# Optimization experiments

Hardware: AMD Instinct MI355X
Metric: run time of the kernel (lower is better)

Reference implementation:

```python
import jax, jax.numpy as jnp
import numpy as np

NUM_NODES = 100000
FVLEN = 256
HDIM = 256
B = 16384
NNEIGH = 32


def setup_inputs() -> dict:
    key = jax.random.key(0)
    k0, k1, k2, k3, k4 = jax.random.split(key, 5)
    x0 = jax.random.randint(k0, (B,), 0, NUM_NODES)
    x1 = jax.random.randint(k1, (B, NNEIGH), 0, NUM_NODES)
    emb = jax.random.normal(k2, (NUM_NODES, FVLEN), dtype=jnp.float32)
    # xavier_uniform-style init for linear weights
    lim = float(np.sqrt(6.0 / (FVLEN + HDIM)))
    W_self = jax.random.uniform(k3, (HDIM, FVLEN), jnp.float32, -lim, lim)
    W_neigh = jax.random.uniform(k4, (HDIM, FVLEN), jnp.float32, -lim, lim)
    b_self = jnp.zeros((HDIM,), jnp.float32)
    b_neigh = jnp.zeros((HDIM,), jnp.float32)
    return {"x0": x0, "x1": x1, "emb": emb, "W_self": W_self,
            "b_self": b_self, "W_neigh": W_neigh, "b_neigh": b_neigh}


def reference(x0, x1, emb, W_self, b_self, W_neigh, b_neigh):
    # gather self features: [B, F]
    self_feats = emb[x0]
    # gather neighbor features and mean-pool over neighbor axis: [B, F]
    neigh_feats = emb[x1].mean(axis=1)
    # dual linear projections (torch Linear: x @ W.T + b)
    self_out = self_feats @ W_self.T + b_self       # [B, H]
    neigh_out = neigh_feats @ W_neigh.T + b_neigh   # [B, H]
    # concat + relu: [B, 2H]
    return jax.nn.relu(jnp.concatenate([self_out, neigh_out], axis=1))
```

## Files before the change

kernel.cpp:

```cpp
#include <hip/hip_runtime.h>

typedef __attribute__((ext_vector_type(4))) float f32x4;
typedef __attribute__((ext_vector_type(8))) short bf16x8;

#define NN 32
#define FV 256

__device__ __forceinline__ unsigned short bf16_rne(float x) {
    unsigned int u = __float_as_uint(x);
    u += 0x7FFFu + ((u >> 16) & 1u);
    return (unsigned short)(u >> 16);
}
__device__ __forceinline__ float bf16_f(unsigned short h) {
    return __uint_as_float(((unsigned int)h) << 16);
}

__global__ __launch_bounds__(256) void pack_weights(
    const float* __restrict__ Wself, const float* __restrict__ Wneigh,
    unsigned short* __restrict__ wpack)
{
    const float* W = blockIdx.y ? Wneigh : Wself;
    unsigned short* hi = wpack + (size_t)blockIdx.y * 131072;
    unsigned short* lo = hi + 65536;
    int t = blockIdx.x * 256 + threadIdx.x;
    int l = t & 63;
    int ks = (t >> 6) & 7;
    int ct = t >> 9;
    int h = ct * 16 + (l & 15);
    int f0 = ks * 32 + ((l >> 4) << 3);
    const float* src = W + h * 256 + f0;
    f32x4 a = *(const f32x4*)src;
    f32x4 b = *(const f32x4*)(src + 4);
    bf16x8 hv, lv;
#pragma unroll
    for (int e = 0; e < 8; ++e) {
        float x = (e < 4) ? a[e] : b[e - 4];
        unsigned short h16 = bf16_rne(x);
        hv[e] = (short)h16;
        lv[e] = (short)bf16_rne(x - bf16_f(h16));
    }
    *(bf16x8*)(hi + (size_t)t * 8) = hv;
    *(bf16x8*)(lo + (size_t)t * 8) = lv;
}

__global__ __launch_bounds__(256) void gather_pool(
    const int* __restrict__ x0, const int* __restrict__ x1,
    const float* __restrict__ emb, float* __restrict__ out)
{
    int b = blockIdx.x;
    int tid = threadIdx.x;
    int g = tid >> 6, l = tid & 63;
    __shared__ f32x4 red[3][64];

    const int* xr = x1 + b * NN;
    int idx[8];
#pragma unroll
    for (int jj = 0; jj < 8; ++jj) idx[jj] = xr[g + jj * 4];

    int sidx = 0;
    if (g == 0) sidx = x0[b];

    f32x4 acc = {0.f, 0.f, 0.f, 0.f};
#pragma unroll
    for (int jj = 0; jj < 8; ++jj) {
        const f32x4* row = (const f32x4*)(emb + (size_t)idx[jj] * FV);
        acc += row[l];
    }
    f32x4 s = {0.f, 0.f, 0.f, 0.f};
    if (g == 0) s = ((const f32x4*)(emb + (size_t)sidx * FV))[l];

    if (g > 0) red[g - 1][l] = acc;
    __syncthreads();
    if (g == 0) {
        f32x4 p = acc + red[0][l] + red[1][l] + red[2][l];
        p *= (1.0f / 32.0f);
        f32x4* o = (f32x4*)(out + (size_t)b * 512);
        o[l] = s;
        o[64 + l] = p;
    }
}

__global__ __launch_bounds__(256) void dual_gemm(
    const float* X, const unsigned short* __restrict__ wpack,
    const float* __restrict__ bias_self, const float* __restrict__ bias_neigh,
    float* out)
{
    __shared__ short Xh[64 * 256];
    __shared__ short Xl[64 * 256];
    int half = blockIdx.y;
    int b0 = blockIdx.x * 64;
    int tid = threadIdx.x;

    const unsigned short* Whi = wpack + (size_t)half * 131072;
    const unsigned short* Wlo = Whi + 65536;
    const float* bias = half ? bias_neigh : bias_self;

#pragma unroll
    for (int it = 0; it < 8; ++it) {
        int c = it * 256 + tid;
        int row = c >> 5;
        int k8 = c & 31;
        const float* src = X + (size_t)(b0 + row) * 512 + half * 256 + k8 * 8;
        f32x4 v0 = *(const f32x4*)src;
        f32x4 v1 = *(const f32x4*)(src + 4);
        bf16x8 hv, lv;
#pragma unroll
        for (int e = 0; e < 8; ++e) {
            float x = (e < 4) ? v0[e] : v1[e - 4];
            unsigned short h16 = bf16_rne(x);
            hv[e] = (short)h16;
            lv[e] = (short)bf16_rne(x - bf16_f(h16));
        }
        int boff = (row * 512 + k8 * 16) ^ ((row & 7) << 4);
        *(bf16x8*)((char*)Xh + boff) = hv;
        *(bf16x8*)((char*)Xl + boff) = lv;
    }
    __syncthreads();

    int w = tid >> 6, l = tid & 63;
    int mh = w & 1;
    int nh = w >> 1;
    int colq = l & 15;
    int kq = l >> 4;

    f32x4 acc[2][8];
#pragma unroll
    for (int c = 0; c < 8; ++c) {
        int ct = nh * 8 + c;
        float bv = bias[ct * 16 + colq];
#pragma unroll
        for (int m = 0; m < 2; ++m) acc[m][c] = {bv, bv, bv, bv};
    }

#pragma unroll
    for (int ks = 0; ks < 8; ++ks) {
        bf16x8 Ah[2], Al[2];
#pragma unroll
        for (int m = 0; m < 2; ++m) {
            int row = mh * 32 + m * 16 + colq;
            int boff = (row * 512 + ks * 64 + (kq << 4)) ^ ((row & 7) << 4);
            Ah[m] = *(const bf16x8*)((const char*)Xh + boff);
            Al[m] = *(const bf16x8*)((const char*)Xl + boff);
        }
#pragma unroll
        for (int c = 0; c < 8; ++c) {
            int ct = nh * 8 + c;
            size_t fo = ((size_t)(ct * 8 + ks) * 64 + l) * 8;
            bf16x8 Bh = *(const bf16x8*)(Whi + fo);
            bf16x8 Bl = *(const bf16x8*)(Wlo + fo);
#pragma unroll
            for (int m = 0; m < 2; ++m) {
                acc[m][c] = __builtin_amdgcn_mfma_f32_16x16x32_bf16(Ah[m], Bh, acc[m][c], 0, 0, 0);
                acc[m][c] = __builtin_amdgcn_mfma_f32_16x16x32_bf16(Al[m], Bh, acc[m][c], 0, 0, 0);
                acc[m][c] = __builtin_amdgcn_mfma_f32_16x16x32_bf16(Ah[m], Bl, acc[m][c], 0, 0, 0);
            }
        }
    }

#pragma unroll
    for (int m = 0; m < 2; ++m) {
        int rb = mh * 32 + m * 16 + (kq << 2);
#pragma unroll
        for (int c = 0; c < 8; ++c) {
            int col = (nh * 8 + c) * 16 + colq;
            float* o = out + (size_t)(b0 + rb) * 512 + half * 256 + col;
#pragma unroll
            for (int j = 0; j < 4; ++j) {
                o[(size_t)j * 512] = fmaxf(acc[m][c][j], 0.0f);
            }
        }
    }
}

extern "C" void kernel_launch(void* const* d_in, const int* in_sizes, int n_in,
                              void* d_out, int out_size, void* d_ws, size_t ws_size,
                              hipStream_t stream) {
    const int* x0 = (const int*)d_in[0];
    const int* x1 = (const int*)d_in[1];
    const float* emb = (const float*)d_in[2];
    const float* Wself = (const float*)d_in[3];
    const float* bself = (const float*)d_in[4];
    const float* Wneigh = (const float*)d_in[5];
    const float* bneigh = (const float*)d_in[6];
    float* out = (float*)d_out;
    unsigned short* wpack = (unsigned short*)d_ws;

    pack_weights<<<dim3(32, 2), 256, 0, stream>>>(Wself, Wneigh, wpack);
    gather_pool<<<16384, 256, 0, stream>>>(x0, x1, emb, out);
    dual_gemm<<<dim3(256, 2), 256, 0, stream>>>(out, wpack, bself, bneigh, out);
}
```

Measured before the change: 246.4 us.

## Split activations into bf16 hi/lo planes in gather and retile GEMM with LDS-staged weights

The gather kernel now writes the pooled and self features as precomputed bf16 hi/lo planes to workspace instead of fp32 into the output buffer. This removes the fp32 re-read and per-block conversion inside the GEMM. A new GEMM kernel uses 512-thread blocks with 256-row tiles, stages a weight slice in LDS, and reads the A operand directly from global memory. The fast path runs only if the workspace is large enough; otherwise it falls back to the old path, and it adds extra workspace traffic for the intermediate planes.

After: 244.9 us. About the same (-0.6%).

```diff
diff --git a/kernel.cpp b/kernel.cpp
--- a/kernel.cpp
+++ b/kernel.cpp
@@ -2,6 +2,7 @@
 
 typedef __attribute__((ext_vector_type(4))) float f32x4;
 typedef __attribute__((ext_vector_type(8))) short bf16x8;
+typedef __attribute__((ext_vector_type(4))) short bf16x4;
 
 #define NN 32
 #define FV 256
@@ -43,9 +44,10 @@
     *(bf16x8*)(lo + (size_t)t * 8) = lv;
 }
 
-__global__ __launch_bounds__(256) void gather_pool(
+__global__ __launch_bounds__(256) void gather_pool_split(
     const int* __restrict__ x0, const int* __restrict__ x1,
-    const float* __restrict__ emb, float* __restrict__ out)
+    const float* __restrict__ emb,
+    unsigned short* __restrict__ Xhi, unsigned short* __restrict__ Xlo)
 {
     int b = blockIdx.x;
     int tid = threadIdx.x;
@@ -74,13 +76,142 @@
     if (g == 0) {
         f32x4 p = acc + red[0][l] + red[1][l] + red[2][l];
         p *= (1.0f / 32.0f);
-        f32x4* o = (f32x4*)(out + (size_t)b * 512);
+        bf16x4 sh, sl, ph, pl;
+#pragma unroll
+        for (int e = 0; e < 4; ++e) {
+            unsigned short h16 = bf16_rne(s[e]);
+            sh[e] = (short)h16;
+            sl[e] = (short)bf16_rne(s[e] - bf16_f(h16));
+            unsigned short h2 = bf16_rne(p[e]);
+            ph[e] = (short)h2;
+            pl[e] = (short)bf16_rne(p[e] - bf16_f(h2));
+        }
+        size_t base = (size_t)b * 512 + l * 4;
+        *(bf16x4*)(Xhi + base)       = sh;
+        *(bf16x4*)(Xlo + base)       = sl;
+        *(bf16x4*)(Xhi + base + 256) = ph;
+        *(bf16x4*)(Xlo + base + 256) = pl;
+    }
+}
+
+__global__ __launch_bounds__(256) void gather_pool(
+    const int* __restrict__ x0, const int* __restrict__ x1,
+    const float* __restrict__ emb, float* __restrict__ xout)
+{
+    int b = blockIdx.x;
+    int tid = threadIdx.x;
+    int g = tid >> 6, l = tid & 63;
+    __shared__ f32x4 red[3][64];
+
+    const int* xr = x1 + b * NN;
+    int idx[8];
+#pragma unroll
+    for (int jj = 0; jj < 8; ++jj) idx[jj] = xr[g + jj * 4];
+
+    int sidx = 0;
+    if (g == 0) sidx = x0[b];
+
+    f32x4 acc = {0.f, 0.f, 0.f, 0.f};
+#pragma unroll
+    for (int jj = 0; jj < 8; ++jj) {
+        const f32x4* row = (const f32x4*)(emb + (size_t)idx[jj] * FV);
+        acc += row[l];
+    }
+    f32x4 s = {0.f, 0.f, 0.f, 0.f};
+    if (g == 0) s = ((const f32x4*)(emb + (size_t)sidx * FV))[l];
+
+    if (g > 0) red[g - 1][l] = acc;
+    __syncthreads();
+    if (g == 0) {
+        f32x4 p = acc + red[0][l] + red[1][l] + red[2][l];
+        p *= (1.0f / 32.0f);
+        f32x4* o = (f32x4*)(xout + (size_t)b * 512);
         o[l] = s;
         o[64 + l] = p;
     }
 }
 
-__global__ __launch_bounds__(256) void dual_gemm(
+__global__ __launch_bounds__(512, 2) void dual_gemm_v3(
+    const unsigned short* __restrict__ Xhi, const unsigned short* __restrict__ Xlo,
+    const unsigned short* __restrict__ wpack,
+    const float* __restrict__ bias_self, const float* __restrict__ bias_neigh,
+    float* __restrict__ out)
+{
+    __shared__ bf16x8 Wlds[2][4096];
+    int mt = blockIdx.x, ns = blockIdx.y, half = blockIdx.z;
+    int b0 = mt * 256;
+    int tid = threadIdx.x;
+
+    const bf16x8* hsrc = (const bf16x8*)(wpack + (size_t)half * 131072 + (size_t)ns * 32768);
+    const bf16x8* lsrc = (const bf16x8*)(wpack + (size_t)half * 131072 + 65536 + (size_t)ns * 32768);
+#pragma unroll
+    for (int it = 0; it < 8; ++it) {
+        int i = it * 512 + tid;
+        Wlds[0][i] = hsrc[i];
+        Wlds[1][i] = lsrc[i];
+    }
+    __syncthreads();
+
+    int w = tid >> 6, l = tid & 63;
+    int mg = w >> 1;
+    int ng = w & 1;
+    int colq = l & 15;
+    int kq = l >> 4;
+
+    const float* bias = half ? bias_neigh : bias_self;
+
+    f32x4 acc[4][4];
+#pragma unroll
+    for (int c = 0; c < 4; ++c) {
+        float bv = bias[(ns * 8 + ng * 4 + c) * 16 + colq];
+#pragma unroll
+        for (int m = 0; m < 4; ++m) acc[m][c] = {bv, bv, bv, bv};
+    }
+
+#pragma unroll
+    for (int ks = 0; ks < 8; ++ks) {
+        bf16x8 Ah[4], Al[4];
+#pragma unroll
+        for (int m = 0; m < 4; ++m) {
+            size_t ao = (size_t)(b0 + mg * 64 + m * 16 + colq) * 512
+                        + half * 256 + ks * 32 + kq * 8;
+            Ah[m] = *(const bf16x8*)(Xhi + ao);
+            Al[m] = *(const bf16x8*)(Xlo + ao);
+        }
+        bf16x8 Bh[4], Bl[4];
+#pragma unroll
+        for (int c = 0; c < 4; ++c) {
+            int bi = (ng * 4 + c) * 512 + ks * 64 + l;
+            Bh[c] = Wlds[0][bi];
+            Bl[c] = Wlds[1][bi];
+        }
+#pragma unroll
+        for (int c = 0; c < 4; ++c) {
+#pragma unroll
+            for (int m = 0; m < 4; ++m) {
+                acc[m][c] = __builtin_amdgcn_mfma_f32_16x16x32_bf16(Ah[m], Bh[c], acc[m][c], 0, 0, 0);
+                acc[m][c] = __builtin_amdgcn_mfma_f32_16x16x32_bf16(Al[m], Bh[c], acc[m][c], 0, 0, 0);
+                acc[m][c] = __builtin_amdgcn_mfma_f32_16x16x32_bf16(Ah[m], Bl[c], acc[m][c], 0, 0, 0);
+            }
+        }
+    }
+
+#pragma unroll
+    for (int m = 0; m < 4; ++m) {
+#pragma unroll
+        for (int c = 0; c < 4; ++c) {
+            int row = b0 + mg * 64 + m * 16 + kq * 4;
+            int col = half * 256 + (ns * 8 + ng * 4 + c) * 16 + colq;
+            float* o = out + (size_t)row * 512 + col;
+#pragma unroll
+            for (int j = 0; j < 4; ++j) {
+                o[(size_t)j * 512] = fmaxf(acc[m][c][j], 0.0f);
+            }
+        }
+    }
+}
+
+__global__ __launch_bounds__(256) void dual_gemm_inplace(
     const float* X, const unsigned short* __restrict__ wpack,
     const float* __restrict__ bias_self, const float* __restrict__ bias_neigh,
     float* out)
@@ -184,8 +315,18 @@
     const float* bneigh = (const float*)d_in[6];
     float* out = (float*)d_out;
     unsigned short* wpack = (unsigned short*)d_ws;
+    const size_t wpack_bytes = 512 * 1024;
+    const size_t xplane_bytes = (size_t)16384 * 512 * 2;
 
     pack_weights<<<dim3(32, 2), 256, 0, stream>>>(Wself, Wneigh, wpack);
-    gather_pool<<<16384, 256, 0, stream>>>(x0, x1, emb, out);
-    dual_gemm<<<dim3(256, 2), 256, 0, stream>>>(out, wpack, bself, bneigh, out);
-}
+
+    if (ws_size >= wpack_bytes + 2 * xplane_bytes) {
+        unsigned short* Xhi = (unsigned short*)((char*)d_ws + wpack_bytes);
+        unsigned short* Xlo = Xhi + (size_t)16384 * 512;
+        gather_pool_split<<<16384, 256, 0, stream>>>(x0, x1, emb, Xhi, Xlo);
+        dual_gemm_v3<<<dim3(64, 2, 2), 512, 0, stream>>>(Xhi, Xlo, wpack, bself, bneigh, out);
+    } else {
+        gather_pool<<<16384, 256, 0, stream>>>(x0, x1, emb, out);
+        dual_gemm_inplace<<<dim3(256, 2), 256, 0, stream>>>(out, wpack, bself, bneigh, out);
+    }
+}
```
